# Kernel tuning notes

Measured on AMD Instinct MI355X. Metric: run time of the kernel, lower is better.

## Reference

```python
import jax, jax.numpy as jnp
import numpy as np

D_MODEL = 1024
NUM_HEADS = 16
D_K = D_MODEL // NUM_HEADS
THETA = 10000.0
BATCH = 2
SEQ = 2048


def apply_rope(x, token_positions):
    # x: [B, H, S, D_K]; token_positions: [S] int
    half = D_K // 2
    inv_freq = THETA ** (-(jnp.arange(half, dtype=jnp.float32) * 2.0) / D_K)  # [half]
    angles = token_positions.astype(jnp.float32)[:, None] * inv_freq[None, :]  # [S, half]
    cos = jnp.cos(angles)  # [S, half]
    sin = jnp.sin(angles)
    x1 = x[..., 0::2]  # even indices
    x2 = x[..., 1::2]  # odd indices
    out_even = x1 * cos - x2 * sin
    out_odd = x1 * sin + x2 * cos
    # interleave back: [..., S, half, 2] -> [..., S, D_K]
    return jnp.stack([out_even, out_odd], axis=-1).reshape(x.shape)


def setup_inputs() -> dict:
    key = jax.random.key(0)
    ks = jax.random.split(key, 5)
    x = jax.random.normal(ks[0], (BATCH, SEQ, D_MODEL), dtype=jnp.float32)
    token_positions = jnp.arange(SEQ, dtype=jnp.int64)
    scale = 0.02
    Wq = jax.random.normal(ks[1], (D_MODEL, D_MODEL), dtype=jnp.float32) * scale
    Wk = jax.random.normal(ks[2], (D_MODEL, D_MODEL), dtype=jnp.float32) * scale
    Wv = jax.random.normal(ks[3], (D_MODEL, D_MODEL), dtype=jnp.float32) * scale
    Wo = jax.random.normal(ks[4], (D_MODEL, D_MODEL), dtype=jnp.float32) * scale
    return {"x": x, "token_positions": token_positions, "Wq": Wq, "Wk": Wk, "Wv": Wv, "Wo": Wo}


def reference(x, token_positions, Wq, Wk, Wv, Wo):
    B, S, _ = x.shape
    # cs336 Linear: y = x @ W.T with W of shape (out, in), no bias
    def proj(W):
        h = jnp.einsum('bsd,od->bso', x, W)
        return h.reshape(B, S, NUM_HEADS, D_K).transpose(0, 2, 1, 3)  # [B,H,S,Dk]
    Q = apply_rope(proj(Wq), token_positions)
    K = apply_rope(proj(Wk), token_positions)
    V = proj(Wv)
    scores = jnp.einsum('bhqd,bhkd->bhqk', Q, K) / jnp.sqrt(jnp.float32(D_K))
    causal = jnp.tril(jnp.ones((S, S), dtype=bool))
    scores = jnp.where(causal, scores, -jnp.inf)
    attn = jax.nn.softmax(scores, axis=-1)
    out = jnp.einsum('bhqk,bhkd->bhqd', attn, V)  # [B,H,S,Dk]
    out = out.transpose(0, 2, 1, 3).reshape(B, S, D_MODEL)
    return jnp.einsum('bsd,od->bso', out, Wo)
```

## Files before the change

### kernel.cpp

```cpp
#include <hip/hip_runtime.h>
#include <hip/hip_bf16.h>
#include <math.h>

#define NHEADS 16
#define DKH 64
#define SEQ 2048
#define DMODEL 1024

typedef __attribute__((ext_vector_type(8))) short short8;
typedef __attribute__((ext_vector_type(4))) float f32x4;

#define GLDS16(g, l)                                         \
  __builtin_amdgcn_global_load_lds(                          \
      (__attribute__((address_space(1))) void*)(void*)(g),   \
      (__attribute__((address_space(3))) void*)(l), 16, 0, 0)

__device__ __forceinline__ short f2bf(float f) {
  unsigned u = __float_as_uint(f);
  unsigned r = (u + 0x7fffu + ((u >> 16) & 1u)) >> 16;
  return (short)r;
}

__device__ __forceinline__ short8 pack8(float4 a, float4 b) {
  short8 v;
  v[0] = f2bf(a.x); v[1] = f2bf(a.y); v[2] = f2bf(a.z); v[3] = f2bf(a.w);
  v[4] = f2bf(b.x); v[5] = f2bf(b.y); v[6] = f2bf(b.z); v[7] = f2bf(b.w);
  return v;
}

__device__ __forceinline__ int swz(int r, int gran) {
  return r * 64 + ((gran ^ (r & 7)) << 3);
}

__global__ __launch_bounds__(256) void precast_rope_kernel(
    const float* __restrict__ X, const float* __restrict__ Wq,
    const float* __restrict__ Wk, const float* __restrict__ Wv,
    const float* __restrict__ Wo, const int* __restrict__ tp,
    short* __restrict__ Xb, short* __restrict__ Wqb, short* __restrict__ Wkb,
    short* __restrict__ Wvb, short* __restrict__ Wob,
    float* __restrict__ ct, float* __restrict__ st) {
  int bid = blockIdx.x;
  if (bid < 4096) {
    int i = bid * 256 + threadIdx.x;
    const float* src; short* dst; int off;
    if (i < 524288) { src = X; dst = Xb; off = i; }
    else {
      int k = i - 524288; int w = k >> 17; off = k & 131071;
      src = (w == 0) ? Wq : (w == 1) ? Wk : (w == 2) ? Wv : Wo;
      dst = (w == 0) ? Wqb : (w == 1) ? Wkb : (w == 2) ? Wvb : Wob;
    }
    const float4* p = reinterpret_cast<const float4*>(src) + 2 * (size_t)off;
    float4 a = p[0], b = p[1];
    reinterpret_cast<short8*>(dst)[off] = pack8(a, b);
  } else {
    int idx = (bid - 4096) * 256 + threadIdx.x;
    if (idx >= SEQ * 32) return;
    int s = idx >> 5, i = idx & 31;
    int is64 = (tp[1] == 0);
    int p = is64 ? tp[2 * s] : tp[s];
    float invf = powf(10000.0f, -(2.0f * (float)i) / 64.0f);
    float a = (float)p * invf;
    ct[idx] = cosf(a);
    st[idx] = sinf(a);
  }
}

__global__ __launch_bounds__(256) void gemm_qkv_kernel(
    const short* __restrict__ X, const short* __restrict__ Wq,
    const short* __restrict__ Wk, const short* __restrict__ Wv,
    short* __restrict__ Qb, short* __restrict__ Kb, short* __restrict__ Vb,
    const float* __restrict__ ct, const float* __restrict__ st) {
  __shared__ __align__(16) short As[128 * 64];
  __shared__ __align__(16) short Bs[128 * 64];
  const int tm = blockIdx.x;
  const int tn = blockIdx.y;
  const int tid = threadIdx.x;
  const int wave = tid >> 6, lane = tid & 63;
  const int l15 = lane & 15, quad = lane >> 4;
  const int wm = wave >> 1, wn = wave & 1;

  const int mid = tn >> 3;
  const int n0 = (tn & 7) * 128;
  const short* W = (mid == 0) ? Wq : (mid == 1 ? Wk : Wv);
  const short* Abase = X + (size_t)(tm * 128) * DMODEL;
  const short* Bbase = W + (size_t)n0 * DMODEL;

  const int lr = lane >> 3;
  const int lc = (lane & 7) ^ lr;

  f32x4 acc[4][4];
#pragma unroll
  for (int mb = 0; mb < 4; mb++)
#pragma unroll
    for (int nb = 0; nb < 4; nb++) acc[mb][nb] = (f32x4){0.f, 0.f, 0.f, 0.f};

  for (int kk = 0; kk < 16; kk++) {
    const short* Ak = Abase + kk * 64;
    const short* Bk = Bbase + kk * 64;
#pragma unroll
    for (int i = 0; i < 4; i++) {
      int R = i * 32 + wave * 8;
      GLDS16(Ak + (size_t)(R + lr) * DMODEL + lc * 8, &As[R * 64 + lane * 8]);
    }
#pragma unroll
    for (int i = 0; i < 4; i++) {
      int R = i * 32 + wave * 8;
      GLDS16(Bk + (size_t)(R + lr) * DMODEL + lc * 8, &Bs[R * 64 + lane * 8]);
    }
    __syncthreads();
#pragma unroll
    for (int kg = 0; kg < 2; kg++) {
      short8 af[4], bf[4];
#pragma unroll
      for (int mb = 0; mb < 4; mb++) {
        int r = wm * 64 + mb * 16 + l15;
        af[mb] = *reinterpret_cast<const short8*>(&As[swz(r, kg * 4 + quad)]);
      }
#pragma unroll
      for (int nb = 0; nb < 4; nb++) {
        int r = wn * 64 + nb * 16 + l15;
        bf[nb] = *reinterpret_cast<const short8*>(&Bs[swz(r, kg * 4 + quad)]);
      }
#pragma unroll
      for (int mb = 0; mb < 4; mb++)
#pragma unroll
        for (int nb = 0; nb < 4; nb++)
          acc[mb][nb] = __builtin_amdgcn_mfma_f32_16x16x32_bf16(af[mb], bf[nb], acc[mb][nb], 0, 0, 0);
    }
    __syncthreads();
  }

#pragma unroll
  for (int mb = 0; mb < 4; mb++) {
    const int s0g = tm * 128 + wm * 64 + mb * 16 + quad * 4;
    const int b = s0g >> 11, s = s0g & 2047;
#pragma unroll
    for (int nb = 0; nb < 4; nb++) {
      int nl = n0 + wn * 64 + nb * 16 + l15;
      int h = nl >> 6, dd = nl & 63;
      if (mid == 2) {
        unsigned u0 = (unsigned)(unsigned short)f2bf(acc[mb][nb][0]) |
                      ((unsigned)(unsigned short)f2bf(acc[mb][nb][1]) << 16);
        unsigned u1 = (unsigned)(unsigned short)f2bf(acc[mb][nb][2]) |
                      ((unsigned)(unsigned short)f2bf(acc[mb][nb][3]) << 16);
        uint2 pk; pk.x = u0; pk.y = u1;
        *reinterpret_cast<uint2*>(Vb + ((size_t)(b * NHEADS + h) * DKH + dd) * SEQ + s) = pk;
      } else {
#pragma unroll
        for (int reg = 0; reg < 4; reg++) {
          float v = acc[mb][nb][reg];
          float pv = __shfl_xor(v, 1);
          int fi = dd >> 1;
          int sg = s + reg;
          float c = ct[sg * 32 + fi], sn = st[sg * 32 + fi];
          float o = (dd & 1) ? (pv * sn + v * c) : (v * c - pv * sn);
          size_t oi = (((size_t)(b * NHEADS + h)) * SEQ + sg) * DKH + dd;
          ((mid == 0) ? Qb : Kb)[oi] = f2bf(o);
        }
      }
    }
  }
}

__global__ __launch_bounds__(256, 4) void attn_kernel(
    const short* __restrict__ Qb, const short* __restrict__ Kb,
    const short* __restrict__ Vtb, short* __restrict__ Ob) {
  __shared__ __align__(16) short QPs[64 * 64];
  __shared__ __align__(16) short Ks[2][64 * 64];
  __shared__ __align__(16) short Vs[2][64 * 64];

  const int id = blockIdx.x;
  const int xx = id & 7;
  const int mm = (((id >> 3) & 3) + (id >> 8)) & 3;
  const int bh = id >> 5;
  const int qt = (mm == 0) ? (31 - xx) : (mm == 1) ? (16 + xx)
               : (mm == 2) ? (15 - xx) : xx;

  const int tid = threadIdx.x;
  const int wave = tid >> 6, lane = tid & 63;
  const int l15 = lane & 15, quad = lane >> 4;
  const int sr0 = tid >> 3, sc = tid & 7;

  const short* Qp = Qb + (size_t)bh * SEQ * DKH;
  const short* Kp = Kb + (size_t)bh * SEQ * DKH;
  const short* Vp = Vtb + (size_t)bh * DKH * SEQ;

  uint4 kreg[2], vreg[2];
#pragma unroll
  for (int i = 0; i < 2; i++) {
    int r = sr0 + i * 32;
    kreg[i] = *reinterpret_cast<const uint4*>(Kp + (size_t)r * DKH + sc * 8);
    vreg[i] = *reinterpret_cast<const uint4*>(Vp + (size_t)r * SEQ + sc * 8);
  }
#pragma unroll
  for (int i = 0; i < 2; i++) {
    int r = sr0 + i * 32;
    uint4 v = *reinterpret_cast<const uint4*>(Qp + (size_t)(qt * 64 + r) * DKH + sc * 8);
    *reinterpret_cast<uint4*>(&QPs[swz(r, sc)]) = v;
  }
#pragma unroll
  for (int i = 0; i < 2; i++) {
    int r = sr0 + i * 32;
    *reinterpret_cast<uint4*>(&Ks[0][swz(r, sc)]) = kreg[i];
    *reinterpret_cast<uint4*>(&Vs[0][swz(r, sc)]) = vreg[i];
  }
  __syncthreads();
  short8 qf0, qf1;
  {
    int r = wave * 16 + l15;
    qf0 = *reinterpret_cast<const short8*>(&QPs[swz(r, quad)]);
    qf1 = *reinterpret_cast<const short8*>(&QPs[swz(r, 4 + quad)]);
  }

  f32x4 accO[4];
#pragma unroll
  for (int i = 0; i < 4; i++) accO[i] = (f32x4){0.f, 0.f, 0.f, 0.f};
  float rs = 0.f;

  const float SCL = 0.125f * 1.44269504089f;
  const float FM = 13.0f;

  int buf = 0;
  for (int kt = 0; kt <= qt; kt++) {
    if (kt < qt) {
#pragma unroll
      for (int i = 0; i < 2; i++) {
        int r = sr0 + i * 32;
        kreg[i] = *reinterpret_cast<const uint4*>(Kp + (size_t)((kt + 1) * 64 + r) * DKH + sc * 8);
        vreg[i] = *reinterpret_cast<const uint4*>(Vp + (size_t)r * SEQ + (kt + 1) * 64 + sc * 8);
      }
    }

    f32x4 sa[4];
#pragma unroll
    for (int nb = 0; nb < 4; nb++) {
      sa[nb] = (f32x4){0.f, 0.f, 0.f, 0.f};
      int r = nb * 16 + l15;
      short8 kf0 = *reinterpret_cast<const short8*>(&Ks[buf][swz(r, quad)]);
      sa[nb] = __builtin_amdgcn_mfma_f32_16x16x32_bf16(kf0, qf0, sa[nb], 0, 0, 0);
      short8 kf1 = *reinterpret_cast<const short8*>(&Ks[buf][swz(r, 4 + quad)]);
      sa[nb] = __builtin_amdgcn_mfma_f32_16x16x32_bf16(kf1, qf1, sa[nb], 0, 0, 0);
    }

    const bool diag = (kt == qt);
    const int prow = wave * 16 + l15;
#pragma unroll
    for (int nb = 0; nb < 4; nb++) {
      float p0 = exp2f(sa[nb][0] * SCL - FM);
      float p1 = exp2f(sa[nb][1] * SCL - FM);
      float p2 = exp2f(sa[nb][2] * SCL - FM);
      float p3 = exp2f(sa[nb][3] * SCL - FM);
      if (diag) {
        int kbase = nb * 16 + quad * 4;
        if (kbase + 0 > prow) p0 = 0.f;
        if (kbase + 1 > prow) p1 = 0.f;
        if (kbase + 2 > prow) p2 = 0.f;
        if (kbase + 3 > prow) p3 = 0.f;
      }
      rs += (p0 + p1) + (p2 + p3);
      unsigned u0 = (unsigned)(unsigned short)f2bf(p0) |
                    ((unsigned)(unsigned short)f2bf(p1) << 16);
      unsigned u1 = (unsigned)(unsigned short)f2bf(p2) |
                    ((unsigned)(unsigned short)f2bf(p3) << 16);
      uint2 pk; pk.x = u0; pk.y = u1;
      int g = 2 * nb + (quad >> 1);
      *reinterpret_cast<uint2*>(&QPs[swz(prow, g) + (quad & 1) * 4]) = pk;
    }

    short8 pf0 = *reinterpret_cast<const short8*>(&QPs[swz(prow, quad)]);
    short8 pf1 = *reinterpret_cast<const short8*>(&QPs[swz(prow, 4 + quad)]);
#pragma unroll
    for (int db = 0; db < 4; db++) {
      int dv = db * 16 + l15;
      short8 vf0 = *reinterpret_cast<const short8*>(&Vs[buf][swz(dv, quad)]);
      accO[db] = __builtin_amdgcn_mfma_f32_16x16x32_bf16(pf0, vf0, accO[db], 0, 0, 0);
      short8 vf1 = *reinterpret_cast<const short8*>(&Vs[buf][swz(dv, 4 + quad)]);
      accO[db] = __builtin_amdgcn_mfma_f32_16x16x32_bf16(pf1, vf1, accO[db], 0, 0, 0);
    }

    if (kt < qt) {
      int nbuf = buf ^ 1;
#pragma unroll
      for (int i = 0; i < 2; i++) {
        int r = sr0 + i * 32;
        *reinterpret_cast<uint4*>(&Ks[nbuf][swz(r, sc)]) = kreg[i];
        *reinterpret_cast<uint4*>(&Vs[nbuf][swz(r, sc)]) = vreg[i];
      }
      __syncthreads();
      buf = nbuf;
    }
  }

  float t = rs;
  t += __shfl_xor(t, 16);
  t += __shfl_xor(t, 32);
  float lv[4];
#pragma unroll
  for (int reg = 0; reg < 4; reg++) lv[reg] = __shfl(t, quad * 4 + reg);

  int b = bh >> 4, h = bh & 15;
#pragma unroll
  for (int db = 0; db < 4; db++)
#pragma unroll
    for (int reg = 0; reg < 4; reg++) {
      int s = qt * 64 + wave * 16 + quad * 4 + reg;
      int dv = db * 16 + l15;
      float o = accO[db][reg] / lv[reg];
      Ob[((size_t)(b * SEQ + s)) * DMODEL + h * DKH + dv] = f2bf(o);
    }
}

__global__ __launch_bounds__(256) void gemm_out_kernel(
    const short* __restrict__ X, const short* __restrict__ Wo, float* __restrict__ Out) {
  __shared__ __align__(16) short As[128 * 64];
  __shared__ __align__(16) short Bs[64 * 64];
  const int tm = blockIdx.x;
  const int tn = blockIdx.y;
  const int tid = threadIdx.x;
  const int wave = tid >> 6, lane = tid & 63;
  const int l15 = lane & 15, quad = lane >> 4;
  const int wm = wave >> 1, wn = wave & 1;

  const short* Abase = X + (size_t)(tm * 128) * DMODEL;
  const short* Bbase = Wo + (size_t)(tn * 64) * DMODEL;

  const int lr = lane >> 3;
  const int lc = (lane & 7) ^ lr;

  f32x4 acc[4][2];
#pragma unroll
  for (int mb = 0; mb < 4; mb++)
#pragma unroll
    for (int nb = 0; nb < 2; nb++) acc[mb][nb] = (f32x4){0.f, 0.f, 0.f, 0.f};

  for (int kk = 0; kk < 16; kk++) {
    const short* Ak = Abase + kk * 64;
    const short* Bk = Bbase + kk * 64;
#pragma unroll
    for (int i = 0; i < 4; i++) {
      int R = i * 32 + wave * 8;
      GLDS16(Ak + (size_t)(R + lr) * DMODEL + lc * 8, &As[R * 64 + lane * 8]);
    }
#pragma unroll
    for (int i = 0; i < 2; i++) {
      int R = i * 32 + wave * 8;
      GLDS16(Bk + (size_t)(R + lr) * DMODEL + lc * 8, &Bs[R * 64 + lane * 8]);
    }
    __syncthreads();
#pragma unroll
    for (int kg = 0; kg < 2; kg++) {
      short8 af[4], bf[2];
#pragma unroll
      for (int mb = 0; mb < 4; mb++) {
        int r = wm * 64 + mb * 16 + l15;
        af[mb] = *reinterpret_cast<const short8*>(&As[swz(r, kg * 4 + quad)]);
      }
#pragma unroll
      for (int nb = 0; nb < 2; nb++) {
        int r = wn * 32 + nb * 16 + l15;
        bf[nb] = *reinterpret_cast<const short8*>(&Bs[swz(r, kg * 4 + quad)]);
      }
#pragma unroll
      for (int mb = 0; mb < 4; mb++)
#pragma unroll
        for (int nb = 0; nb < 2; nb++)
          acc[mb][nb] = __builtin_amdgcn_mfma_f32_16x16x32_bf16(af[mb], bf[nb], acc[mb][nb], 0, 0, 0);
    }
    __syncthreads();
  }
#pragma unroll
  for (int mb = 0; mb < 4; mb++)
#pragma unroll
    for (int nb = 0; nb < 2; nb++)
#pragma unroll
      for (int reg = 0; reg < 4; reg++) {
        int rg = tm * 128 + wm * 64 + mb * 16 + quad * 4 + reg;
        int col = tn * 64 + wn * 32 + nb * 16 + l15;
        Out[(size_t)rg * DMODEL + col] = acc[mb][nb][reg];
      }
}

extern "C" void kernel_launch(void* const* d_in, const int* in_sizes, int n_in,
                              void* d_out, int out_size, void* d_ws, size_t ws_size,
                              hipStream_t stream) {
  (void)in_sizes; (void)n_in; (void)out_size; (void)ws_size;
  const float* X  = (const float*)d_in[0];
  const int*   tp = (const int*)d_in[1];
  const float* Wq = (const float*)d_in[2];
  const float* Wk = (const float*)d_in[3];
  const float* Wv = (const float*)d_in[4];
  const float* Wo = (const float*)d_in[5];
  float* Out = (float*)d_out;

  short* Qb  = (short*)d_ws;
  short* Kb  = Qb + 4194304;
  short* Vb  = Kb + 4194304;
  short* Ab  = Vb + 4194304;
  short* Xb  = Ab + 4194304;
  short* Wqb = Xb + 4194304;
  short* Wkb = Wqb + 1048576;
  short* Wvb = Wkb + 1048576;
  short* Wob = Wvb + 1048576;
  float* ct  = (float*)(Wob + 1048576);
  float* st  = ct + SEQ * 32;

  precast_rope_kernel<<<dim3(4352), dim3(256), 0, stream>>>(
      X, Wq, Wk, Wv, Wo, tp, Xb, Wqb, Wkb, Wvb, Wob, ct, st);
  gemm_qkv_kernel<<<dim3(32, 24), dim3(256), 0, stream>>>(Xb, Wqb, Wkb, Wvb,
                                                          Qb, Kb, Vb, ct, st);
  attn_kernel<<<dim3(1024), dim3(256), 0, stream>>>(Qb, Kb, Vb, Ab);
  gemm_out_kernel<<<dim3(32, 16), dim3(256), 0, stream>>>(Ab, Wob, Out);
}
```

Baseline: 190.9 us.

## Restructure QKV GEMM into 256x256 tiles with double-buffered LDS pipeline

The QKV projection GEMM moves from 128x128 tiles with 256 threads to 256x256 tiles with 512 threads. LDS is now double-buffered, with the next k-slice loaded via global_load_lds while MFMAs run, and explicit vmcnt waits, barriers and setprio interleave loads with compute. B fragments are held in registers across four A sub-phases. The intent is to hide global load latency and raise data reuse per tile. In exchange it uses more LDS and registers, and launches far fewer blocks (192 instead of 768), which may leave CUs idle.

Result: slower. 195.9 us (+2.6%).

```diff
diff --git a/kernel.cpp b/kernel.cpp
--- a/kernel.cpp
+++ b/kernel.cpp
@@ -65,90 +65,128 @@
   }
 }
 
-__global__ __launch_bounds__(256) void gemm_qkv_kernel(
+__global__ __launch_bounds__(512, 2) void gemm_qkv_kernel(
     const short* __restrict__ X, const short* __restrict__ Wq,
     const short* __restrict__ Wk, const short* __restrict__ Wv,
     short* __restrict__ Qb, short* __restrict__ Kb, short* __restrict__ Vb,
     const float* __restrict__ ct, const float* __restrict__ st) {
-  __shared__ __align__(16) short As[128 * 64];
-  __shared__ __align__(16) short Bs[128 * 64];
+  __shared__ __align__(16) short As[2][256 * 64];
+  __shared__ __align__(16) short Bs[2][256 * 64];
   const int tm = blockIdx.x;
   const int tn = blockIdx.y;
   const int tid = threadIdx.x;
   const int wave = tid >> 6, lane = tid & 63;
   const int l15 = lane & 15, quad = lane >> 4;
-  const int wm = wave >> 1, wn = wave & 1;
-
-  const int mid = tn >> 3;
-  const int n0 = (tn & 7) * 128;
+  const int wm = wave >> 2, wn = wave & 3;
+
+  const int mid = tn >> 2;
+  const int n0 = (tn & 3) * 256;
   const short* W = (mid == 0) ? Wq : (mid == 1 ? Wk : Wv);
-  const short* Abase = X + (size_t)(tm * 128) * DMODEL;
+  const short* Abase = X + (size_t)(tm * 256) * DMODEL;
   const short* Bbase = W + (size_t)n0 * DMODEL;
 
   const int lr = lane >> 3;
   const int lc = (lane & 7) ^ lr;
 
-  f32x4 acc[4][4];
-#pragma unroll
-  for (int mb = 0; mb < 4; mb++)
-#pragma unroll
-    for (int nb = 0; nb < 4; nb++) acc[mb][nb] = (f32x4){0.f, 0.f, 0.f, 0.f};
-
-  for (int kk = 0; kk < 16; kk++) {
-    const short* Ak = Abase + kk * 64;
-    const short* Bk = Bbase + kk * 64;
-#pragma unroll
-    for (int i = 0; i < 4; i++) {
-      int R = i * 32 + wave * 8;
-      GLDS16(Ak + (size_t)(R + lr) * DMODEL + lc * 8, &As[R * 64 + lane * 8]);
-    }
-#pragma unroll
-    for (int i = 0; i < 4; i++) {
-      int R = i * 32 + wave * 8;
-      GLDS16(Bk + (size_t)(R + lr) * DMODEL + lc * 8, &Bs[R * 64 + lane * 8]);
-    }
-    __syncthreads();
-#pragma unroll
-    for (int kg = 0; kg < 2; kg++) {
-      short8 af[4], bf[4];
-#pragma unroll
-      for (int mb = 0; mb < 4; mb++) {
-        int r = wm * 64 + mb * 16 + l15;
-        af[mb] = *reinterpret_cast<const short8*>(&As[swz(r, kg * 4 + quad)]);
-      }
-#pragma unroll
-      for (int nb = 0; nb < 4; nb++) {
-        int r = wn * 64 + nb * 16 + l15;
-        bf[nb] = *reinterpret_cast<const short8*>(&Bs[swz(r, kg * 4 + quad)]);
-      }
-#pragma unroll
-      for (int mb = 0; mb < 4; mb++)
+#define STG(SRC, DST, bufi, half, kt_)                                     \
+  do {                                                                     \
+    int R0 = (half) * 128 + wave * 16;                                     \
+    GLDS16((SRC) + (size_t)(R0 + lr) * DMODEL + (kt_) * 64 + lc * 8,       \
+           &DST[bufi][R0 * 64 + lane * 8]);                                \
+    GLDS16((SRC) + (size_t)(R0 + 8 + lr) * DMODEL + (kt_) * 64 + lc * 8,   \
+           &DST[bufi][(R0 + 8) * 64 + lane * 8]);                          \
+  } while (0)
+
+  f32x4 acc[8][4];
+#pragma unroll
+  for (int m = 0; m < 8; m++)
+#pragma unroll
+    for (int n = 0; n < 4; n++) acc[m][n] = (f32x4){0.f, 0.f, 0.f, 0.f};
+
+  STG(Bbase, Bs, 0, 0, 0); STG(Bbase, Bs, 0, 1, 0);
+  STG(Abase, As, 0, 0, 0); STG(Abase, As, 0, 1, 0);
+  STG(Bbase, Bs, 1, 0, 1); STG(Bbase, Bs, 1, 1, 1);
+
+  short8 bfr[4][2];
+  for (int kt = 0; kt < 16; kt++) {
+    const int buf = kt & 1;
+    if (kt < 15) { STG(Abase, As, buf ^ 1, 0, kt + 1); }
+    if (kt < 15) { asm volatile("s_waitcnt vmcnt(6)" ::: "memory"); }
+    else         { asm volatile("s_waitcnt vmcnt(0)" ::: "memory"); }
+    asm volatile("s_barrier" ::: "memory");
+#pragma unroll
+    for (int nb = 0; nb < 4; nb++)
+#pragma unroll
+      for (int ks = 0; ks < 2; ks++)
+        bfr[nb][ks] = *reinterpret_cast<const short8*>(
+            &Bs[buf][swz(wn * 64 + nb * 16 + l15, ks * 4 + quad)]);
+    {
+      short8 af[2][2];
+#pragma unroll
+      for (int j = 0; j < 2; j++)
+#pragma unroll
+        for (int ks = 0; ks < 2; ks++)
+          af[j][ks] = *reinterpret_cast<const short8*>(
+              &As[buf][swz(wm * 128 + j * 16 + l15, ks * 4 + quad)]);
+      __builtin_amdgcn_s_setprio(1);
+#pragma unroll
+      for (int j = 0; j < 2; j++)
 #pragma unroll
         for (int nb = 0; nb < 4; nb++)
-          acc[mb][nb] = __builtin_amdgcn_mfma_f32_16x16x32_bf16(af[mb], bf[nb], acc[mb][nb], 0, 0, 0);
-    }
-    __syncthreads();
-  }
-
-#pragma unroll
-  for (int mb = 0; mb < 4; mb++) {
-    const int s0g = tm * 128 + wm * 64 + mb * 16 + quad * 4;
+#pragma unroll
+          for (int ks = 0; ks < 2; ks++)
+            acc[j][nb] = __builtin_amdgcn_mfma_f32_16x16x32_bf16(
+                af[j][ks], bfr[nb][ks], acc[j][nb], 0, 0, 0);
+      __builtin_amdgcn_s_setprio(0);
+    }
+    asm volatile("s_barrier" ::: "memory");
+#pragma unroll
+    for (int p = 1; p < 4; p++) {
+      short8 af[2][2];
+#pragma unroll
+      for (int j = 0; j < 2; j++)
+#pragma unroll
+        for (int ks = 0; ks < 2; ks++)
+          af[j][ks] = *reinterpret_cast<const short8*>(
+              &As[buf][swz(wm * 128 + (p * 2 + j) * 16 + l15, ks * 4 + quad)]);
+      if (p == 1)      { if (kt < 15) { STG(Abase, As, buf ^ 1, 1, kt + 1); } }
+      else if (p == 2) { if (kt < 14) { STG(Bbase, Bs, buf, 0, kt + 2); } }
+      else             { if (kt < 14) { STG(Bbase, Bs, buf, 1, kt + 2); } }
+      asm volatile("s_barrier" ::: "memory");
+      __builtin_amdgcn_s_setprio(1);
+#pragma unroll
+      for (int j = 0; j < 2; j++)
+#pragma unroll
+        for (int nb = 0; nb < 4; nb++)
+#pragma unroll
+          for (int ks = 0; ks < 2; ks++)
+            acc[p * 2 + j][nb] = __builtin_amdgcn_mfma_f32_16x16x32_bf16(
+                af[j][ks], bfr[nb][ks], acc[p * 2 + j][nb], 0, 0, 0);
+      __builtin_amdgcn_s_setprio(0);
+      asm volatile("s_barrier" ::: "memory");
+    }
+  }
+#undef STG
+
+#pragma unroll
+  for (int mf = 0; mf < 8; mf++) {
+    const int s0g = tm * 256 + wm * 128 + mf * 16 + quad * 4;
     const int b = s0g >> 11, s = s0g & 2047;
 #pragma unroll
     for (int nb = 0; nb < 4; nb++) {
       int nl = n0 + wn * 64 + nb * 16 + l15;
       int h = nl >> 6, dd = nl & 63;
       if (mid == 2) {
-        unsigned u0 = (unsigned)(unsigned short)f2bf(acc[mb][nb][0]) |
-                      ((unsigned)(unsigned short)f2bf(acc[mb][nb][1]) << 16);
-        unsigned u1 = (unsigned)(unsigned short)f2bf(acc[mb][nb][2]) |
-                      ((unsigned)(unsigned short)f2bf(acc[mb][nb][3]) << 16);
+        unsigned u0 = (unsigned)(unsigned short)f2bf(acc[mf][nb][0]) |
+                      ((unsigned)(unsigned short)f2bf(acc[mf][nb][1]) << 16);
+        unsigned u1 = (unsigned)(unsigned short)f2bf(acc[mf][nb][2]) |
+                      ((unsigned)(unsigned short)f2bf(acc[mf][nb][3]) << 16);
         uint2 pk; pk.x = u0; pk.y = u1;
         *reinterpret_cast<uint2*>(Vb + ((size_t)(b * NHEADS + h) * DKH + dd) * SEQ + s) = pk;
       } else {
 #pragma unroll
         for (int reg = 0; reg < 4; reg++) {
-          float v = acc[mb][nb][reg];
+          float v = acc[mf][nb][reg];
           float pv = __shfl_xor(v, 1);
           int fi = dd >> 1;
           int sg = s + reg;
@@ -406,7 +444,7 @@
 
   precast_rope_kernel<<<dim3(4352), dim3(256), 0, stream>>>(
       X, Wq, Wk, Wv, Wo, tp, Xb, Wqb, Wkb, Wvb, Wob, ct, st);
-  gemm_qkv_kernel<<<dim3(32, 24), dim3(256), 0, stream>>>(Xb, Wqb, Wkb, Wvb,
+  gemm_qkv_kernel<<<dim3(16, 12), dim3(512), 0, stream>>>(Xb, Wqb, Wkb, Wvb,
                                                           Qb, Kb, Vb, ct, st);
   attn_kernel<<<dim3(1024), dim3(256), 0, stream>>>(Qb, Kb, Vb, Ab);
   gemm_out_kernel<<<dim3(32, 16), dim3(256), 0, stream>>>(Ab, Wob, Out);
```

## Keep P in registers, double query tile per block, permute V LDS layout

Applied to the files above, without the earlier changes.

The attention kernel now processes 128 query rows per block (two 16-row groups per wave) instead of 64. Each loaded K/V tile is reused for twice as many queries, and the grid is halved with a new causal load-balancing map. The P matrix is no longer staged through shared memory: the V tile is stored in a permuted layout so the MFMA output registers of P can feed the PV MFMA directly after packing with v_cvt_pk_bf16_f32. Q fragments are loaded straight from global memory, and s_setprio is raised around the MFMA blocks. This raises register pressure (launch bounds drop to 2 blocks per CU) and leaves fewer blocks to balance across CUs.

Result: slower. 195.7 us (+2.5%).

```diff
diff --git a/kernel.cpp b/kernel.cpp
--- a/kernel.cpp
+++ b/kernel.cpp
@@ -19,6 +19,12 @@
   unsigned u = __float_as_uint(f);
   unsigned r = (u + 0x7fffu + ((u >> 16) & 1u)) >> 16;
   return (short)r;
+}
+
+__device__ __forceinline__ unsigned cvtpk(float lo, float hi) {
+  unsigned r;
+  asm("v_cvt_pk_bf16_f32 %0, %1, %2" : "=v"(r) : "v"(lo), "v"(hi));
+  return r;
 }
 
 __device__ __forceinline__ short8 pack8(float4 a, float4 b) {
@@ -162,25 +168,28 @@
   }
 }
 
-__global__ __launch_bounds__(256, 4) void attn_kernel(
+__global__ __launch_bounds__(256, 2) void attn_kernel(
     const short* __restrict__ Qb, const short* __restrict__ Kb,
     const short* __restrict__ Vtb, short* __restrict__ Ob) {
-  __shared__ __align__(16) short QPs[64 * 64];
   __shared__ __align__(16) short Ks[2][64 * 64];
   __shared__ __align__(16) short Vs[2][64 * 64];
 
   const int id = blockIdx.x;
-  const int xx = id & 7;
-  const int mm = (((id >> 3) & 3) + (id >> 8)) & 3;
-  const int bh = id >> 5;
-  const int qt = (mm == 0) ? (31 - xx) : (mm == 1) ? (16 + xx)
-               : (mm == 2) ? (15 - xx) : xx;
+  const int x8 = id & 7;
+  const int c  = (id >> 3) & 31;
+  const int rr = id >> 8;
+  const int bh = x8 * 4 + (c >> 4) * 2 + rr;
+  const int qt = rr ? (15 - (c & 15)) : (c & 15);
+  const int ntiles = 2 * qt + 2;
 
   const int tid = threadIdx.x;
   const int wave = tid >> 6, lane = tid & 63;
   const int l15 = lane & 15, quad = lane >> 4;
   const int sr0 = tid >> 3, sc = tid & 7;
 
+  const int vga = ((sc >> 2) << 2) + ((sc & 1) << 1);
+  const int vh4 = ((sc >> 1) & 1) * 4;
+
   const short* Qp = Qb + (size_t)bh * SEQ * DKH;
   const short* Kp = Kb + (size_t)bh * SEQ * DKH;
   const short* Vp = Vtb + (size_t)bh * DKH * SEQ;
@@ -192,37 +201,37 @@
     kreg[i] = *reinterpret_cast<const uint4*>(Kp + (size_t)r * DKH + sc * 8);
     vreg[i] = *reinterpret_cast<const uint4*>(Vp + (size_t)r * SEQ + sc * 8);
   }
-#pragma unroll
-  for (int i = 0; i < 2; i++) {
-    int r = sr0 + i * 32;
-    uint4 v = *reinterpret_cast<const uint4*>(Qp + (size_t)(qt * 64 + r) * DKH + sc * 8);
-    *reinterpret_cast<uint4*>(&QPs[swz(r, sc)]) = v;
+  short8 qf[2][2];
+#pragma unroll
+  for (int g = 0; g < 2; g++) {
+    const short* qrow = Qp + (size_t)(qt * 128 + wave * 32 + g * 16 + l15) * DKH;
+    qf[g][0] = *reinterpret_cast<const short8*>(qrow + quad * 8);
+    qf[g][1] = *reinterpret_cast<const short8*>(qrow + (4 + quad) * 8);
   }
 #pragma unroll
   for (int i = 0; i < 2; i++) {
     int r = sr0 + i * 32;
     *reinterpret_cast<uint4*>(&Ks[0][swz(r, sc)]) = kreg[i];
-    *reinterpret_cast<uint4*>(&Vs[0][swz(r, sc)]) = vreg[i];
+    uint2 lo, hi;
+    lo.x = vreg[i].x; lo.y = vreg[i].y; hi.x = vreg[i].z; hi.y = vreg[i].w;
+    *reinterpret_cast<uint2*>(&Vs[0][swz(r, vga) + vh4]) = lo;
+    *reinterpret_cast<uint2*>(&Vs[0][swz(r, vga + 1) + vh4]) = hi;
   }
   __syncthreads();
-  short8 qf0, qf1;
-  {
-    int r = wave * 16 + l15;
-    qf0 = *reinterpret_cast<const short8*>(&QPs[swz(r, quad)]);
-    qf1 = *reinterpret_cast<const short8*>(&QPs[swz(r, 4 + quad)]);
-  }
-
-  f32x4 accO[4];
-#pragma unroll
-  for (int i = 0; i < 4; i++) accO[i] = (f32x4){0.f, 0.f, 0.f, 0.f};
-  float rs = 0.f;
+
+  f32x4 accO[2][4];
+#pragma unroll
+  for (int g = 0; g < 2; g++)
+#pragma unroll
+    for (int i = 0; i < 4; i++) accO[g][i] = (f32x4){0.f, 0.f, 0.f, 0.f};
+  float rs[2] = {0.f, 0.f};
 
   const float SCL = 0.125f * 1.44269504089f;
   const float FM = 13.0f;
 
   int buf = 0;
-  for (int kt = 0; kt <= qt; kt++) {
-    if (kt < qt) {
+  for (int kt = 0; kt < ntiles; kt++) {
+    if (kt + 1 < ntiles) {
 #pragma unroll
       for (int i = 0; i < 2; i++) {
         int r = sr0 + i * 32;
@@ -231,83 +240,102 @@
       }
     }
 
-    f32x4 sa[4];
+    f32x4 sa[2][4];
+    __builtin_amdgcn_s_setprio(1);
 #pragma unroll
     for (int nb = 0; nb < 4; nb++) {
-      sa[nb] = (f32x4){0.f, 0.f, 0.f, 0.f};
       int r = nb * 16 + l15;
       short8 kf0 = *reinterpret_cast<const short8*>(&Ks[buf][swz(r, quad)]);
-      sa[nb] = __builtin_amdgcn_mfma_f32_16x16x32_bf16(kf0, qf0, sa[nb], 0, 0, 0);
       short8 kf1 = *reinterpret_cast<const short8*>(&Ks[buf][swz(r, 4 + quad)]);
-      sa[nb] = __builtin_amdgcn_mfma_f32_16x16x32_bf16(kf1, qf1, sa[nb], 0, 0, 0);
-    }
-
-    const bool diag = (kt == qt);
-    const int prow = wave * 16 + l15;
-#pragma unroll
-    for (int nb = 0; nb < 4; nb++) {
-      float p0 = exp2f(sa[nb][0] * SCL - FM);
-      float p1 = exp2f(sa[nb][1] * SCL - FM);
-      float p2 = exp2f(sa[nb][2] * SCL - FM);
-      float p3 = exp2f(sa[nb][3] * SCL - FM);
-      if (diag) {
-        int kbase = nb * 16 + quad * 4;
-        if (kbase + 0 > prow) p0 = 0.f;
-        if (kbase + 1 > prow) p1 = 0.f;
-        if (kbase + 2 > prow) p2 = 0.f;
-        if (kbase + 3 > prow) p3 = 0.f;
-      }
-      rs += (p0 + p1) + (p2 + p3);
-      unsigned u0 = (unsigned)(unsigned short)f2bf(p0) |
-                    ((unsigned)(unsigned short)f2bf(p1) << 16);
-      unsigned u1 = (unsigned)(unsigned short)f2bf(p2) |
-                    ((unsigned)(unsigned short)f2bf(p3) << 16);
-      uint2 pk; pk.x = u0; pk.y = u1;
-      int g = 2 * nb + (quad >> 1);
-      *reinterpret_cast<uint2*>(&QPs[swz(prow, g) + (quad & 1) * 4]) = pk;
-    }
-
-    short8 pf0 = *reinterpret_cast<const short8*>(&QPs[swz(prow, quad)]);
-    short8 pf1 = *reinterpret_cast<const short8*>(&QPs[swz(prow, 4 + quad)]);
+      sa[0][nb] = (f32x4){0.f, 0.f, 0.f, 0.f};
+      sa[0][nb] = __builtin_amdgcn_mfma_f32_16x16x32_bf16(kf0, qf[0][0], sa[0][nb], 0, 0, 0);
+      sa[0][nb] = __builtin_amdgcn_mfma_f32_16x16x32_bf16(kf1, qf[0][1], sa[0][nb], 0, 0, 0);
+      sa[1][nb] = (f32x4){0.f, 0.f, 0.f, 0.f};
+      sa[1][nb] = __builtin_amdgcn_mfma_f32_16x16x32_bf16(kf0, qf[1][0], sa[1][nb], 0, 0, 0);
+      sa[1][nb] = __builtin_amdgcn_mfma_f32_16x16x32_bf16(kf1, qf[1][1], sa[1][nb], 0, 0, 0);
+    }
+    __builtin_amdgcn_s_setprio(0);
+
+    const bool diag = (kt >= 2 * qt);
+    unsigned pu[2][4], pw[2][4];
+#pragma unroll
+    for (int g = 0; g < 2; g++) {
+      const int rrel = qt * 128 + wave * 32 + g * 16 + l15 - kt * 64;
+#pragma unroll
+      for (int nb = 0; nb < 4; nb++) {
+        float p0 = exp2f(sa[g][nb][0] * SCL - FM);
+        float p1 = exp2f(sa[g][nb][1] * SCL - FM);
+        float p2 = exp2f(sa[g][nb][2] * SCL - FM);
+        float p3 = exp2f(sa[g][nb][3] * SCL - FM);
+        if (diag) {
+          int kbase = nb * 16 + quad * 4;
+          if (kbase + 0 > rrel) p0 = 0.f;
+          if (kbase + 1 > rrel) p1 = 0.f;
+          if (kbase + 2 > rrel) p2 = 0.f;
+          if (kbase + 3 > rrel) p3 = 0.f;
+        }
+        rs[g] += (p0 + p1) + (p2 + p3);
+        pu[g][nb] = cvtpk(p0, p1);
+        pw[g][nb] = cvtpk(p2, p3);
+      }
+    }
+
+    short8 pf[2][2];
+#pragma unroll
+    for (int g = 0; g < 2; g++) {
+      unsigned* w0 = reinterpret_cast<unsigned*>(&pf[g][0]);
+      w0[0] = pu[g][0]; w0[1] = pw[g][0]; w0[2] = pu[g][1]; w0[3] = pw[g][1];
+      unsigned* w1 = reinterpret_cast<unsigned*>(&pf[g][1]);
+      w1[0] = pu[g][2]; w1[1] = pw[g][2]; w1[2] = pu[g][3]; w1[3] = pw[g][3];
+    }
+    __builtin_amdgcn_s_setprio(1);
 #pragma unroll
     for (int db = 0; db < 4; db++) {
       int dv = db * 16 + l15;
       short8 vf0 = *reinterpret_cast<const short8*>(&Vs[buf][swz(dv, quad)]);
-      accO[db] = __builtin_amdgcn_mfma_f32_16x16x32_bf16(pf0, vf0, accO[db], 0, 0, 0);
       short8 vf1 = *reinterpret_cast<const short8*>(&Vs[buf][swz(dv, 4 + quad)]);
-      accO[db] = __builtin_amdgcn_mfma_f32_16x16x32_bf16(pf1, vf1, accO[db], 0, 0, 0);
-    }
-
-    if (kt < qt) {
+      accO[0][db] = __builtin_amdgcn_mfma_f32_16x16x32_bf16(pf[0][0], vf0, accO[0][db], 0, 0, 0);
+      accO[0][db] = __builtin_amdgcn_mfma_f32_16x16x32_bf16(pf[0][1], vf1, accO[0][db], 0, 0, 0);
+      accO[1][db] = __builtin_amdgcn_mfma_f32_16x16x32_bf16(pf[1][0], vf0, accO[1][db], 0, 0, 0);
+      accO[1][db] = __builtin_amdgcn_mfma_f32_16x16x32_bf16(pf[1][1], vf1, accO[1][db], 0, 0, 0);
+    }
+    __builtin_amdgcn_s_setprio(0);
+
+    if (kt + 1 < ntiles) {
       int nbuf = buf ^ 1;
 #pragma unroll
       for (int i = 0; i < 2; i++) {
         int r = sr0 + i * 32;
         *reinterpret_cast<uint4*>(&Ks[nbuf][swz(r, sc)]) = kreg[i];
-        *reinterpret_cast<uint4*>(&Vs[nbuf][swz(r, sc)]) = vreg[i];
+        uint2 lo, hi;
+        lo.x = vreg[i].x; lo.y = vreg[i].y; hi.x = vreg[i].z; hi.y = vreg[i].w;
+        *reinterpret_cast<uint2*>(&Vs[nbuf][swz(r, vga) + vh4]) = lo;
+        *reinterpret_cast<uint2*>(&Vs[nbuf][swz(r, vga + 1) + vh4]) = hi;
       }
       __syncthreads();
       buf = nbuf;
     }
   }
 
-  float t = rs;
-  t += __shfl_xor(t, 16);
-  t += __shfl_xor(t, 32);
-  float lv[4];
-#pragma unroll
-  for (int reg = 0; reg < 4; reg++) lv[reg] = __shfl(t, quad * 4 + reg);
-
   int b = bh >> 4, h = bh & 15;
 #pragma unroll
-  for (int db = 0; db < 4; db++)
-#pragma unroll
-    for (int reg = 0; reg < 4; reg++) {
-      int s = qt * 64 + wave * 16 + quad * 4 + reg;
-      int dv = db * 16 + l15;
-      float o = accO[db][reg] / lv[reg];
-      Ob[((size_t)(b * SEQ + s)) * DMODEL + h * DKH + dv] = f2bf(o);
-    }
+  for (int g = 0; g < 2; g++) {
+    float t = rs[g];
+    t += __shfl_xor(t, 16);
+    t += __shfl_xor(t, 32);
+    float lv[4];
+#pragma unroll
+    for (int reg = 0; reg < 4; reg++) lv[reg] = __shfl(t, quad * 4 + reg);
+#pragma unroll
+    for (int db = 0; db < 4; db++)
+#pragma unroll
+      for (int reg = 0; reg < 4; reg++) {
+        int s = qt * 128 + wave * 32 + g * 16 + quad * 4 + reg;
+        int dv = db * 16 + l15;
+        float o = accO[g][db][reg] / lv[reg];
+        Ob[((size_t)(b * SEQ + s)) * DMODEL + h * DKH + dv] = f2bf(o);
+      }
+  }
 }
 
 __global__ __launch_bounds__(256) void gemm_out_kernel(
@@ -408,6 +436,6 @@
       X, Wq, Wk, Wv, Wo, tp, Xb, Wqb, Wkb, Wvb, Wob, ct, st);
   gemm_qkv_kernel<<<dim3(32, 24), dim3(256), 0, stream>>>(Xb, Wqb, Wkb, Wvb,
                                                           Qb, Kb, Vb, ct, st);
-  attn_kernel<<<dim3(1024), dim3(256), 0, stream>>>(Qb, Kb, Vb, Ab);
+  attn_kernel<<<dim3(512), dim3(256), 0, stream>>>(Qb, Kb, Vb, Ab);
   gemm_out_kernel<<<dim3(32, 16), dim3(256), 0, stream>>>(Ab, Wob, Out);
 }
```
